# Kernel optimization log

Hardware: AMD Instinct MI355X
Metric: run time of the kernel (lower is better)

The kernel has to match this reference:

```python
import jax, jax.numpy as jnp
import numpy as np

N_NODES = 100000
N_EDGES = 1600000
IN_DIM = 64
OUT_DIM = 64
T_STEPS = 4
W_SCALE = 0.01


def setup_inputs() -> dict:
    key = jax.random.key(0)
    k0, k1, k2, k3, k4, k5 = jax.random.split(key, 6)
    Xv = jax.random.normal(k0, (N_NODES, IN_DIM), dtype=jnp.float32)
    edge_index = jax.random.randint(k1, (2, N_EDGES), 0, N_NODES, dtype=jnp.int64)
    W1 = jax.random.normal(k2, (OUT_DIM, IN_DIM), dtype=jnp.float32) * W_SCALE
    W2 = jax.random.normal(k3, (OUT_DIM, OUT_DIM), dtype=jnp.float32) * W_SCALE
    W3 = jax.random.normal(k4, (OUT_DIM, OUT_DIM), dtype=jnp.float32) * W_SCALE
    W4 = jax.random.normal(k5, (OUT_DIM, 1), dtype=jnp.float32) * W_SCALE
    return {"Xv": Xv, "edge_index": edge_index, "W1": W1, "W2": W2, "W3": W3, "W4": W4}


def reference(Xv, edge_index, W1, W2, W3, W4):
    n = Xv.shape[0]
    row = edge_index[0]
    col = edge_index[1]
    # Dense A (all-ones COO, duplicates summed) passed through W4 -> ReLU -> sum over axis 1:
    # sum_j relu(A_ij * w4) = sum_j A_ij * relu(w4)  (ReLU is positively homogeneous, A_ij >= 0)
    #                       = deg_i * relu(w4)
    deg = jax.ops.segment_sum(jnp.ones(row.shape, Xv.dtype), row, num_segments=n)  # [N]
    w4 = W4[:, 0]  # [D]
    v3 = (deg[:, None] * jax.nn.relu(w4)[None, :]) @ W3.T  # [N, D]
    base = Xv @ W1.T + v3  # loop-invariant part (recomputed each step in original, same value)
    emb = jnp.zeros((n, W1.shape[0]), Xv.dtype)
    for _ in range(T_STEPS):
        # sparse A @ emb: gather source embeddings, scatter-add into destination rows
        neigh = jax.ops.segment_sum(emb[col], row, num_segments=n)  # [N, D]
        emb = jax.nn.relu(base + neigh @ W2.T)
    return emb
```

## Files before the change

kernel.cpp:

```cpp
#include <hip/hip_runtime.h>

#define NN 100000
#define NE 1600000
#define D  64
#define BSH 8
#define NBKT ((NN + 255) >> BSH)
#define NBLK_E ((NE / 4 + 1023) / 1024)
#define H_SCALE 256.0f
#define H_ISCALE 0.00390625f

typedef __attribute__((ext_vector_type(8))) short short8v;
typedef __attribute__((ext_vector_type(4))) unsigned short ushort4v;
typedef __attribute__((ext_vector_type(4))) float f32x4;
typedef __attribute__((ext_vector_type(2))) float f32x2;

__device__ __forceinline__ float bf2f(unsigned short x) {
    return __uint_as_float(((unsigned)x) << 16);
}
__device__ __forceinline__ unsigned short f2bf(float f) {
    unsigned u = __float_as_uint(f);
    return (unsigned short)((u + 0x7fff + ((u >> 16) & 1)) >> 16);
}

__global__ __launch_bounds__(256) void k_prep(
        const float* __restrict__ W1, const float* __restrict__ W2,
        const float* __restrict__ W3, const float* __restrict__ W4,
        unsigned short* __restrict__ w1b, unsigned short* __restrict__ w2b,
        float* __restrict__ cvec, int* __restrict__ ghist) {
    int b = blockIdx.x, tid = threadIdx.x;
    if (b < 16) {
        int i = b * 256 + tid;
        w1b[i] = f2bf(W1[i]);
        w2b[i] = f2bf(W2[i]);
    } else {
        for (int i = tid; i < NBKT; i += 256) ghist[i] = 0;
        if (tid < 64) {
            float s = 0.f;
            for (int k = 0; k < D; ++k) {
                float w4 = W4[k];
                s += W3[tid * D + k] * (w4 > 0.f ? w4 : 0.f);
            }
            cvec[tid] = s;
        }
    }
}

__global__ __launch_bounds__(256) void k_hist(const int* __restrict__ row,
                                              int* __restrict__ ghist) {
    __shared__ int h[NBKT];
    int tid = threadIdx.x;
    for (int i = tid; i < NBKT; i += 256) h[i] = 0;
    __syncthreads();
    int base4 = blockIdx.x * 1024;
    #pragma unroll
    for (int k = 0; k < 4; ++k) {
        int i4 = base4 + k * 256 + tid;
        if (i4 < NE / 4) {
            int4 r = ((const int4*)row)[i4];
            atomicAdd(&h[r.x >> BSH], 1);
            atomicAdd(&h[r.y >> BSH], 1);
            atomicAdd(&h[r.z >> BSH], 1);
            atomicAdd(&h[r.w >> BSH], 1);
        }
    }
    __syncthreads();
    for (int i = tid; i < NBKT; i += 256) if (h[i]) atomicAdd(&ghist[i], h[i]);
}

__global__ __launch_bounds__(256) void k_bscan(const int* __restrict__ ghist,
                                               int* __restrict__ bbase,
                                               int* __restrict__ bcur) {
    __shared__ int sc[2][512];
    int t = threadIdx.x;
    int cur = 0;
    #pragma unroll
    for (int k = 0; k < 2; ++k) {
        int i = t + k * 256;
        sc[0][i] = (i < NBKT) ? ghist[i] : 0;
    }
    __syncthreads();
    for (int s = 1; s < 512; s <<= 1) {
        #pragma unroll
        for (int k = 0; k < 2; ++k) {
            int i = t + k * 256;
            sc[cur ^ 1][i] = sc[cur][i] + ((i >= s) ? sc[cur][i - s] : 0);
        }
        cur ^= 1;
        __syncthreads();
    }
    #pragma unroll
    for (int k = 0; k < 2; ++k) {
        int i = t + k * 256;
        if (i < NBKT) {
            int b = (i == 0) ? 0 : sc[cur][i - 1];
            bbase[i] = b;
            bcur[i] = b;
        } else if (i == NBKT) {
            bbase[NBKT] = sc[cur][NBKT - 1];
        }
    }
}

__global__ __launch_bounds__(256) void k_bucket(const int* __restrict__ row,
                                                const int* __restrict__ col,
                                                int* __restrict__ bcur,
                                                unsigned* __restrict__ sorted) {
    __shared__ int hist[NBKT];
    __shared__ int bbase_s[NBKT];
    int tid = threadIdx.x;
    for (int i = tid; i < NBKT; i += 256) hist[i] = 0;
    __syncthreads();
    int base4 = blockIdx.x * 1024;
    int4 r4[4], c4[4];
    int rank[16];
    bool valid[4];
    #pragma unroll
    for (int k = 0; k < 4; ++k) {
        int i4 = base4 + k * 256 + tid;
        valid[k] = (i4 < NE / 4);
        if (valid[k]) {
            r4[k] = ((const int4*)row)[i4];
            c4[k] = ((const int4*)col)[i4];
            rank[k * 4 + 0] = atomicAdd(&hist[r4[k].x >> BSH], 1);
            rank[k * 4 + 1] = atomicAdd(&hist[r4[k].y >> BSH], 1);
            rank[k * 4 + 2] = atomicAdd(&hist[r4[k].z >> BSH], 1);
            rank[k * 4 + 3] = atomicAdd(&hist[r4[k].w >> BSH], 1);
        }
    }
    __syncthreads();
    for (int i = tid; i < NBKT; i += 256)
        bbase_s[i] = hist[i] ? atomicAdd(&bcur[i], hist[i]) : 0;
    __syncthreads();
    #pragma unroll
    for (int k = 0; k < 4; ++k) {
        if (valid[k]) {
            int rr[4] = {r4[k].x, r4[k].y, r4[k].z, r4[k].w};
            int cc[4] = {c4[k].x, c4[k].y, c4[k].z, c4[k].w};
            #pragma unroll
            for (int j = 0; j < 4; ++j) {
                int b = rr[j] >> BSH;
                unsigned pk = ((unsigned)(rr[j] & 255) << 17) | (unsigned)cc[j];
                sorted[bbase_s[b] + rank[k * 4 + j]] = pk;
            }
        }
    }
}

__global__ __launch_bounds__(256) void k_fine(const unsigned* __restrict__ sorted,
                                              const int* __restrict__ bbase,
                                              int* __restrict__ csr_col,
                                              int* __restrict__ cnt_g,
                                              int2* __restrict__ se_g) {
    __shared__ int cnt_s[256];
    __shared__ int cur_s[256];
    __shared__ int sc[2][256];
    int b = blockIdx.x;
    int tid = threadIdx.x;
    int s0 = bbase[b], e0 = bbase[b + 1];
    cnt_s[tid] = 0;
    __syncthreads();
    for (int i = s0 + tid; i < e0; i += 256)
        atomicAdd(&cnt_s[sorted[i] >> 17], 1);
    __syncthreads();
    int cur = 0;
    sc[0][tid] = cnt_s[tid];
    __syncthreads();
    for (int s = 1; s < 256; s <<= 1) {
        sc[cur ^ 1][tid] = sc[cur][tid] + ((tid >= s) ? sc[cur][tid - s] : 0);
        cur ^= 1;
        __syncthreads();
    }
    int incl = sc[cur][tid];
    cur_s[tid] = incl - cnt_s[tid];
    int nb = NN - b * 256;
    nb = nb > 256 ? 256 : nb;
    if (tid < nb) {
        int node = b * 256 + tid;
        cnt_g[node] = cnt_s[tid];
        se_g[node] = make_int2(s0 + incl - cnt_s[tid], s0 + incl);
    }
    __syncthreads();
    for (int i = s0 + tid; i < e0; i += 256) {
        unsigned u = sorted[i];
        int p = atomicAdd(&cur_s[u >> 17], 1);
        csr_col[s0 + p] = (int)(u & 0x1FFFFu);
    }
}

__global__ __launch_bounds__(256) void k_baseh(
        const float* __restrict__ Xv, const unsigned short* __restrict__ w1b,
        const unsigned short* __restrict__ w2b,
        const int* __restrict__ cnt, const float* __restrict__ cvec,
        unsigned short* __restrict__ base_bf, unsigned short* __restrict__ emb_bf,
        unsigned char* __restrict__ h8) {
    __shared__ unsigned short etile[4][16][72];
    int wv = threadIdx.x >> 6;
    int wid = blockIdx.x * 4 + wv;
    int lane = threadIdx.x & 63;
    int m0 = wid * 16;
    if (m0 >= NN) return;
    int r = lane & 15, half = lane >> 4;
    const float* arow = Xv + (size_t)(m0 + r) * D + half * 8;
    f32x4 xa = *(const f32x4*)(arow);
    f32x4 xb = *(const f32x4*)(arow + 4);
    f32x4 xc = *(const f32x4*)(arow + 32);
    f32x4 xd = *(const f32x4*)(arow + 36);
    short8v a0, a1;
    #pragma unroll
    for (int j = 0; j < 4; ++j) {
        a0[j]     = (short)f2bf(xa[j]);
        a0[j + 4] = (short)f2bf(xb[j]);
        a1[j]     = (short)f2bf(xc[j]);
        a1[j + 4] = (short)f2bf(xd[j]);
    }
    int4 c4 = *(const int4*)(cnt + m0 + half * 4);
    float dg[4] = {(float)c4.x, (float)c4.y, (float)c4.z, (float)c4.w};
    #pragma unroll
    for (int t = 0; t < 4; ++t) {
        short8v b0 = *(const short8v*)(w1b + (size_t)(t * 16 + r) * D + half * 8);
        short8v b1 = *(const short8v*)(w1b + (size_t)(t * 16 + r) * D + 32 + half * 8);
        f32x4 cacc = {0.f, 0.f, 0.f, 0.f};
        cacc = __builtin_amdgcn_mfma_f32_16x16x32_bf16(a0, b0, cacc, 0, 0, 0);
        cacc = __builtin_amdgcn_mfma_f32_16x16x32_bf16(a1, b1, cacc, 0, 0, 0);
        float cv = cvec[t * 16 + r];
        #pragma unroll
        for (int q = 0; q < 4; ++q) {
            float s = cacc[q] + dg[q] * cv;
            size_t idx = (size_t)(m0 + half * 4 + q) * D + t * 16 + r;
            unsigned short ebf = f2bf(s > 0.f ? s : 0.f);
            base_bf[idx] = f2bf(s);
            emb_bf[idx] = ebf;
            etile[wv][half * 4 + q][t * 16 + r] = ebf;
        }
    }
    short8v ha0 = *(const short8v*)(&etile[wv][r][half * 8]);
    short8v ha1 = *(const short8v*)(&etile[wv][r][32 + half * 8]);
    #pragma unroll
    for (int t = 0; t < 4; ++t) {
        short8v b0 = *(const short8v*)(w2b + (size_t)(t * 16 + r) * D + half * 8);
        short8v b1 = *(const short8v*)(w2b + (size_t)(t * 16 + r) * D + 32 + half * 8);
        f32x4 cacc = {0.f, 0.f, 0.f, 0.f};
        cacc = __builtin_amdgcn_mfma_f32_16x16x32_bf16(ha0, b0, cacc, 0, 0, 0);
        cacc = __builtin_amdgcn_mfma_f32_16x16x32_bf16(ha1, b1, cacc, 0, 0, 0);
        #pragma unroll
        for (int q = 0; q < 4; ++q) {
            int pk = __builtin_amdgcn_cvt_pk_fp8_f32(cacc[q] * H_SCALE, 0.f, 0, false);
            h8[(size_t)(m0 + half * 4 + q) * D + t * 16 + r] = (unsigned char)(pk & 0xff);
        }
    }
}

__global__ __launch_bounds__(256) void k_h(
        const unsigned short* __restrict__ emb_bf, const unsigned short* __restrict__ w2b,
        unsigned char* __restrict__ h8) {
    int wid = blockIdx.x * 4 + (threadIdx.x >> 6);
    int lane = threadIdx.x & 63;
    int m0 = wid * 16;
    if (m0 >= NN) return;
    int r = lane & 15, half = lane >> 4;
    const unsigned short* arow = emb_bf + (size_t)(m0 + r) * D + half * 8;
    short8v a0 = *(const short8v*)(arow);
    short8v a1 = *(const short8v*)(arow + 32);
    #pragma unroll
    for (int t = 0; t < 4; ++t) {
        short8v b0 = *(const short8v*)(w2b + (size_t)(t * 16 + r) * D + half * 8);
        short8v b1 = *(const short8v*)(w2b + (size_t)(t * 16 + r) * D + 32 + half * 8);
        f32x4 cacc = {0.f, 0.f, 0.f, 0.f};
        cacc = __builtin_amdgcn_mfma_f32_16x16x32_bf16(a0, b0, cacc, 0, 0, 0);
        cacc = __builtin_amdgcn_mfma_f32_16x16x32_bf16(a1, b1, cacc, 0, 0, 0);
        #pragma unroll
        for (int q = 0; q < 4; ++q) {
            int pk = __builtin_amdgcn_cvt_pk_fp8_f32(cacc[q] * H_SCALE, 0.f, 0, false);
            h8[(size_t)(m0 + half * 4 + q) * D + t * 16 + r] = (unsigned char)(pk & 0xff);
        }
    }
}

template<int LAST>
__global__ __launch_bounds__(256) void k_pull(
        const int2* __restrict__ se_g,
        const int* __restrict__ csr_col, const unsigned char* __restrict__ h8,
        const unsigned short* __restrict__ base_bf,
        unsigned short* __restrict__ out_bf, float* __restrict__ out_f32) {
    int tid = threadIdx.x;
    int wave = tid >> 6, lane = tid & 63;
    int q = lane >> 4, l = lane & 15;
    for (int it = blockIdx.x; it < NN / 4; it += gridDim.x) {
        int node = it * 4 + wave;
        int2 se = se_g[node];
        int start = se.x, end = se.y;
        float a0 = 0.f, a1 = 0.f, a2 = 0.f, a3 = 0.f;
        for (int j = start; j < end; j += 16) {
            int e0 = j + q;
            int e1 = j + 4 + q;
            int e2 = j + 8 + q;
            int e3 = j + 12 + q;
            int c0 = (e0 < end) ? csr_col[e0] : -1;
            int c1 = (e1 < end) ? csr_col[e1] : -1;
            int c2 = (e2 < end) ? csr_col[e2] : -1;
            int c3 = (e3 < end) ? csr_col[e3] : -1;
            unsigned v0 = 0, v1 = 0, v2 = 0, v3 = 0;
            if (c0 >= 0) v0 = *((const unsigned*)(h8 + (size_t)c0 * D) + l);
            if (c1 >= 0) v1 = *((const unsigned*)(h8 + (size_t)c1 * D) + l);
            if (c2 >= 0) v2 = *((const unsigned*)(h8 + (size_t)c2 * D) + l);
            if (c3 >= 0) v3 = *((const unsigned*)(h8 + (size_t)c3 * D) + l);
            if (c0 >= 0) {
                f32x2 f0 = __builtin_amdgcn_cvt_pk_f32_fp8(v0, false);
                f32x2 f1 = __builtin_amdgcn_cvt_pk_f32_fp8(v0, true);
                a0 += f0.x; a1 += f0.y; a2 += f1.x; a3 += f1.y;
            }
            if (c1 >= 0) {
                f32x2 f0 = __builtin_amdgcn_cvt_pk_f32_fp8(v1, false);
                f32x2 f1 = __builtin_amdgcn_cvt_pk_f32_fp8(v1, true);
                a0 += f0.x; a1 += f0.y; a2 += f1.x; a3 += f1.y;
            }
            if (c2 >= 0) {
                f32x2 f0 = __builtin_amdgcn_cvt_pk_f32_fp8(v2, false);
                f32x2 f1 = __builtin_amdgcn_cvt_pk_f32_fp8(v2, true);
                a0 += f0.x; a1 += f0.y; a2 += f1.x; a3 += f1.y;
            }
            if (c3 >= 0) {
                f32x2 f0 = __builtin_amdgcn_cvt_pk_f32_fp8(v3, false);
                f32x2 f1 = __builtin_amdgcn_cvt_pk_f32_fp8(v3, true);
                a0 += f0.x; a1 += f0.y; a2 += f1.x; a3 += f1.y;
            }
        }
        a0 += __shfl_xor(a0, 16); a1 += __shfl_xor(a1, 16);
        a2 += __shfl_xor(a2, 16); a3 += __shfl_xor(a3, 16);
        a0 += __shfl_xor(a0, 32); a1 += __shfl_xor(a1, 32);
        a2 += __shfl_xor(a2, 32); a3 += __shfl_xor(a3, 32);
        if (q == 0) {
            ushort4v b4 = *(const ushort4v*)(base_bf + (size_t)node * D + l * 4);
            float r0 = fmaxf(fmaf(a0, H_ISCALE, bf2f(b4[0])), 0.f);
            float r1 = fmaxf(fmaf(a1, H_ISCALE, bf2f(b4[1])), 0.f);
            float r2 = fmaxf(fmaf(a2, H_ISCALE, bf2f(b4[2])), 0.f);
            float r3 = fmaxf(fmaf(a3, H_ISCALE, bf2f(b4[3])), 0.f);
            if (LAST) {
                f32x4 o4 = {r0, r1, r2, r3};
                *(f32x4*)(out_f32 + (size_t)node * D + l * 4) = o4;
            } else {
                ushort4v o4 = {f2bf(r0), f2bf(r1), f2bf(r2), f2bf(r3)};
                *(ushort4v*)(out_bf + (size_t)node * D + l * 4) = o4;
            }
        }
    }
}

extern "C" void kernel_launch(void* const* d_in, const int* in_sizes, int n_in,
                              void* d_out, int out_size, void* d_ws, size_t ws_size,
                              hipStream_t stream) {
    const float* Xv = (const float*)d_in[0];
    const int*   ei = (const int*)d_in[1];
    const float* W1 = (const float*)d_in[2];
    const float* W2 = (const float*)d_in[3];
    const float* W3 = (const float*)d_in[4];
    const float* W4 = (const float*)d_in[5];

    char* ws = (char*)d_ws;
    size_t off = 0;
    unsigned short* base_bf = (unsigned short*)(ws + off); off += (size_t)NN * D * 2;
    unsigned char* h8 = (unsigned char*)(ws + off);    off += (size_t)NN * D;
    int* csr_col = (int*)(ws + off);                   off += (size_t)NE * 4;
    int* cnt     = (int*)(ws + off);                   off += (size_t)NN * 4;
    int2* se_g   = (int2*)(ws + off);                  off += (size_t)NN * 8;
    int* ghist   = (int*)(ws + off);                   off += NBKT * 4;
    int* bbase   = (int*)(ws + off);                   off += (NBKT + 1) * 4;
    int* bcur    = (int*)(ws + off);                   off += NBKT * 4;
    float* cvec  = (float*)(ws + off);                 off += D * 4;
    unsigned short* w1b = (unsigned short*)(ws + off); off += D * D * 2;
    unsigned short* w2b = (unsigned short*)(ws + off); off += D * D * 2;
    unsigned* sorted = (unsigned*)(ws + off);          off += (size_t)NE * 4;

    unsigned short* emb_bf = (unsigned short*)d_out;
    float* emb_f32 = (float*)d_out;

    const int* row = ei;
    const int* col = ei + NE;

    k_prep<<<17, 256, 0, stream>>>(W1, W2, W3, W4, w1b, w2b, cvec, ghist);
    k_hist<<<NBLK_E, 256, 0, stream>>>(row, ghist);
    k_bscan<<<1, 256, 0, stream>>>(ghist, bbase, bcur);
    k_bucket<<<NBLK_E, 256, 0, stream>>>(row, col, bcur, sorted);
    k_fine<<<NBKT, 256, 0, stream>>>(sorted, bbase, csr_col, cnt, se_g);

    k_baseh<<<(NN / 16 + 3) / 4, 256, 0, stream>>>(Xv, w1b, w2b, cnt, cvec,
                                                   base_bf, emb_bf, h8);

    for (int t = 0; t < 3; ++t) {
        if (t > 0)
            k_h<<<(NN / 16 + 3) / 4, 256, 0, stream>>>(emb_bf, w2b, h8);
        if (t < 2)
            k_pull<0><<<2048, 256, 0, stream>>>(se_g, csr_col, h8, base_bf, emb_bf, nullptr);
        else
            k_pull<1><<<2048, 256, 0, stream>>>(se_g, csr_col, h8, base_bf, nullptr, emb_f32);
    }
}
```

Before: 208.0 us.

## Fuse W2 projection into pull kernel with ping-pong fp8 buffers

Merges the separate per-step W2 matmul kernel into the neighbor-aggregation kernel. Each block now aggregates 16 nodes, stages their bf16 embeddings in shared memory, and runs the MFMA projection to write the next fp8 h buffer. Two h buffers are used alternately. This removes the intermediate bf16 embedding write/read and two kernel launches. The grid changes from a persistent 2048-block loop to one block per 16 nodes, and all lanes now load base.

```diff
diff --git a/kernel.cpp b/kernel.cpp
--- a/kernel.cpp
+++ b/kernel.cpp
@@ -191,8 +191,7 @@
         const float* __restrict__ Xv, const unsigned short* __restrict__ w1b,
         const unsigned short* __restrict__ w2b,
         const int* __restrict__ cnt, const float* __restrict__ cvec,
-        unsigned short* __restrict__ base_bf, unsigned short* __restrict__ emb_bf,
-        unsigned char* __restrict__ h8) {
+        unsigned short* __restrict__ base_bf, unsigned char* __restrict__ h8) {
     __shared__ unsigned short etile[4][16][72];
     int wv = threadIdx.x >> 6;
     int wid = blockIdx.x * 4 + wv;
@@ -227,10 +226,8 @@
         for (int q = 0; q < 4; ++q) {
             float s = cacc[q] + dg[q] * cv;
             size_t idx = (size_t)(m0 + half * 4 + q) * D + t * 16 + r;
-            unsigned short ebf = f2bf(s > 0.f ? s : 0.f);
             base_bf[idx] = f2bf(s);
-            emb_bf[idx] = ebf;
-            etile[wv][half * 4 + q][t * 16 + r] = ebf;
+            etile[wv][half * 4 + q][t * 16 + r] = f2bf(s > 0.f ? s : 0.f);
         }
     }
     short8v ha0 = *(const short8v*)(&etile[wv][r][half * 8]);
@@ -250,43 +247,21 @@
     }
 }
 
-__global__ __launch_bounds__(256) void k_h(
-        const unsigned short* __restrict__ emb_bf, const unsigned short* __restrict__ w2b,
-        unsigned char* __restrict__ h8) {
-    int wid = blockIdx.x * 4 + (threadIdx.x >> 6);
-    int lane = threadIdx.x & 63;
-    int m0 = wid * 16;
-    if (m0 >= NN) return;
-    int r = lane & 15, half = lane >> 4;
-    const unsigned short* arow = emb_bf + (size_t)(m0 + r) * D + half * 8;
-    short8v a0 = *(const short8v*)(arow);
-    short8v a1 = *(const short8v*)(arow + 32);
-    #pragma unroll
-    for (int t = 0; t < 4; ++t) {
-        short8v b0 = *(const short8v*)(w2b + (size_t)(t * 16 + r) * D + half * 8);
-        short8v b1 = *(const short8v*)(w2b + (size_t)(t * 16 + r) * D + 32 + half * 8);
-        f32x4 cacc = {0.f, 0.f, 0.f, 0.f};
-        cacc = __builtin_amdgcn_mfma_f32_16x16x32_bf16(a0, b0, cacc, 0, 0, 0);
-        cacc = __builtin_amdgcn_mfma_f32_16x16x32_bf16(a1, b1, cacc, 0, 0, 0);
-        #pragma unroll
-        for (int q = 0; q < 4; ++q) {
-            int pk = __builtin_amdgcn_cvt_pk_fp8_f32(cacc[q] * H_SCALE, 0.f, 0, false);
-            h8[(size_t)(m0 + half * 4 + q) * D + t * 16 + r] = (unsigned char)(pk & 0xff);
-        }
-    }
-}
-
 template<int LAST>
-__global__ __launch_bounds__(256) void k_pull(
+__global__ __launch_bounds__(256) void k_pullh(
         const int2* __restrict__ se_g,
-        const int* __restrict__ csr_col, const unsigned char* __restrict__ h8,
+        const int* __restrict__ csr_col, const unsigned char* __restrict__ h_in,
         const unsigned short* __restrict__ base_bf,
-        unsigned short* __restrict__ out_bf, float* __restrict__ out_f32) {
+        const unsigned short* __restrict__ w2b,
+        unsigned char* __restrict__ h_out, float* __restrict__ out_f32) {
+    __shared__ unsigned short etile[16][72];
     int tid = threadIdx.x;
-    int wave = tid >> 6, lane = tid & 63;
+    int wv = tid >> 6, lane = tid & 63;
     int q = lane >> 4, l = lane & 15;
-    for (int it = blockIdx.x; it < NN / 4; it += gridDim.x) {
-        int node = it * 4 + wave;
+    int m0 = blockIdx.x * 16;
+    #pragma unroll
+    for (int s = 0; s < 4; ++s) {
+        int node = m0 + wv * 4 + s;
         int2 se = se_g[node];
         int start = se.x, end = se.y;
         float a0 = 0.f, a1 = 0.f, a2 = 0.f, a3 = 0.f;
@@ -300,10 +275,10 @@
             int c2 = (e2 < end) ? csr_col[e2] : -1;
             int c3 = (e3 < end) ? csr_col[e3] : -1;
             unsigned v0 = 0, v1 = 0, v2 = 0, v3 = 0;
-            if (c0 >= 0) v0 = *((const unsigned*)(h8 + (size_t)c0 * D) + l);
-            if (c1 >= 0) v1 = *((const unsigned*)(h8 + (size_t)c1 * D) + l);
-            if (c2 >= 0) v2 = *((const unsigned*)(h8 + (size_t)c2 * D) + l);
-            if (c3 >= 0) v3 = *((const unsigned*)(h8 + (size_t)c3 * D) + l);
+            if (c0 >= 0) v0 = *((const unsigned*)(h_in + (size_t)c0 * D) + l);
+            if (c1 >= 0) v1 = *((const unsigned*)(h_in + (size_t)c1 * D) + l);
+            if (c2 >= 0) v2 = *((const unsigned*)(h_in + (size_t)c2 * D) + l);
+            if (c3 >= 0) v3 = *((const unsigned*)(h_in + (size_t)c3 * D) + l);
             if (c0 >= 0) {
                 f32x2 f0 = __builtin_amdgcn_cvt_pk_f32_fp8(v0, false);
                 f32x2 f1 = __builtin_amdgcn_cvt_pk_f32_fp8(v0, true);
@@ -329,19 +304,38 @@
         a2 += __shfl_xor(a2, 16); a3 += __shfl_xor(a3, 16);
         a0 += __shfl_xor(a0, 32); a1 += __shfl_xor(a1, 32);
         a2 += __shfl_xor(a2, 32); a3 += __shfl_xor(a3, 32);
-        if (q == 0) {
-            ushort4v b4 = *(const ushort4v*)(base_bf + (size_t)node * D + l * 4);
-            float r0 = fmaxf(fmaf(a0, H_ISCALE, bf2f(b4[0])), 0.f);
-            float r1 = fmaxf(fmaf(a1, H_ISCALE, bf2f(b4[1])), 0.f);
-            float r2 = fmaxf(fmaf(a2, H_ISCALE, bf2f(b4[2])), 0.f);
-            float r3 = fmaxf(fmaf(a3, H_ISCALE, bf2f(b4[3])), 0.f);
-            if (LAST) {
+        ushort4v b4 = *(const ushort4v*)(base_bf + (size_t)node * D + l * 4);
+        float r0 = fmaxf(fmaf(a0, H_ISCALE, bf2f(b4[0])), 0.f);
+        float r1 = fmaxf(fmaf(a1, H_ISCALE, bf2f(b4[1])), 0.f);
+        float r2 = fmaxf(fmaf(a2, H_ISCALE, bf2f(b4[2])), 0.f);
+        float r3 = fmaxf(fmaf(a3, H_ISCALE, bf2f(b4[3])), 0.f);
+        if (LAST) {
+            if (q == 0) {
                 f32x4 o4 = {r0, r1, r2, r3};
                 *(f32x4*)(out_f32 + (size_t)node * D + l * 4) = o4;
-            } else {
+            }
+        } else {
+            if (q == 0) {
                 ushort4v o4 = {f2bf(r0), f2bf(r1), f2bf(r2), f2bf(r3)};
-                *(ushort4v*)(out_bf + (size_t)node * D + l * 4) = o4;
-            }
+                *(ushort4v*)(&etile[wv * 4 + s][l * 4]) = o4;
+            }
+        }
+    }
+    if (!LAST) {
+        __syncthreads();
+        int r = lane & 15, half = lane >> 4;
+        short8v ha0 = *(const short8v*)(&etile[r][half * 8]);
+        short8v ha1 = *(const short8v*)(&etile[r][32 + half * 8]);
+        int t = wv;
+        short8v b0 = *(const short8v*)(w2b + (size_t)(t * 16 + r) * D + half * 8);
+        short8v b1 = *(const short8v*)(w2b + (size_t)(t * 16 + r) * D + 32 + half * 8);
+        f32x4 cacc = {0.f, 0.f, 0.f, 0.f};
+        cacc = __builtin_amdgcn_mfma_f32_16x16x32_bf16(ha0, b0, cacc, 0, 0, 0);
+        cacc = __builtin_amdgcn_mfma_f32_16x16x32_bf16(ha1, b1, cacc, 0, 0, 0);
+        #pragma unroll
+        for (int qq = 0; qq < 4; ++qq) {
+            int pk = __builtin_amdgcn_cvt_pk_fp8_f32(cacc[qq] * H_SCALE, 0.f, 0, false);
+            h_out[(size_t)(m0 + half * 4 + qq) * D + t * 16 + r] = (unsigned char)(pk & 0xff);
         }
     }
 }
@@ -359,7 +353,8 @@
     char* ws = (char*)d_ws;
     size_t off = 0;
     unsigned short* base_bf = (unsigned short*)(ws + off); off += (size_t)NN * D * 2;
-    unsigned char* h8 = (unsigned char*)(ws + off);    off += (size_t)NN * D;
+    unsigned char* h8a = (unsigned char*)(ws + off);   off += (size_t)NN * D;
+    unsigned char* h8b = (unsigned char*)(ws + off);   off += (size_t)NN * D;
     int* csr_col = (int*)(ws + off);                   off += (size_t)NE * 4;
     int* cnt     = (int*)(ws + off);                   off += (size_t)NN * 4;
     int2* se_g   = (int2*)(ws + off);                  off += (size_t)NN * 8;
@@ -371,7 +366,6 @@
     unsigned short* w2b = (unsigned short*)(ws + off); off += D * D * 2;
     unsigned* sorted = (unsigned*)(ws + off);          off += (size_t)NE * 4;
 
-    unsigned short* emb_bf = (unsigned short*)d_out;
     float* emb_f32 = (float*)d_out;
 
     const int* row = ei;
@@ -384,14 +378,9 @@
     k_fine<<<NBKT, 256, 0, stream>>>(sorted, bbase, csr_col, cnt, se_g);
 
     k_baseh<<<(NN / 16 + 3) / 4, 256, 0, stream>>>(Xv, w1b, w2b, cnt, cvec,
-                                                   base_bf, emb_bf, h8);
-
-    for (int t = 0; t < 3; ++t) {
-        if (t > 0)
-            k_h<<<(NN / 16 + 3) / 4, 256, 0, stream>>>(emb_bf, w2b, h8);
-        if (t < 2)
-            k_pull<0><<<2048, 256, 0, stream>>>(se_g, csr_col, h8, base_bf, emb_bf, nullptr);
-        else
-            k_pull<1><<<2048, 256, 0, stream>>>(se_g, csr_col, h8, base_bf, nullptr, emb_f32);
-    }
-}
+                                                   base_bf, h8a);
+
+    k_pullh<0><<<NN / 16, 256, 0, stream>>>(se_g, csr_col, h8a, base_bf, w2b, h8b, nullptr);
+    k_pullh<0><<<NN / 16, 256, 0, stream>>>(se_g, csr_col, h8b, base_bf, w2b, h8a, nullptr);
+    k_pullh<1><<<NN / 16, 256, 0, stream>>>(se_g, csr_col, h8a, base_bf, w2b, nullptr, emb_f32);
+}
```

New measurement: 201.2 us. 3.3% less time.
